# Optimization experiments

Measured on AMD Instinct MI355X. Metric: run time of the kernel, lower is better.

## Reference

```python
import jax, jax.numpy as jnp
import numpy as np

H = 16        # num_heads
NB = 64       # n_buckets
NH = 6        # n_hyperplanes = log2(NB)


def setup_inputs() -> dict:
    key = jax.random.key(0)
    k = jax.random.split(key, 6)
    E = 1024
    B, S = 2, 2048
    return {
        "x": jax.random.normal(k[0], (B, S, E), jnp.float32),
        "Wq": jax.random.normal(k[1], (E, E), jnp.float32) * (E ** -0.5),
        "bq": jax.random.normal(k[2], (E,), jnp.float32) * 0.02,
        "Wv": jax.random.normal(k[3], (E, E), jnp.float32) * (E ** -0.5),
        "bv": jax.random.normal(k[4], (E,), jnp.float32) * 0.02,
        "hyperplanes": jax.random.normal(k[5], (E // H + 1, NH), jnp.float32),
    }


def reference(x, Wq, bq, Wv, bv, hyperplanes):
    B, S, E = x.shape
    Dh = E // H
    # projections (torch Linear: x @ W.T + b)
    q = (x @ Wq.T + bq).reshape(B, S, H, Dh)
    v = (x @ Wv.T + bv).reshape(B, S, H, Dh)

    # LSH buckets from q: append a ones column, sign-project onto hyperplanes
    qa = jnp.concatenate([q, jnp.ones((B, S, H, 1), q.dtype)], axis=-1)  # [B,S,H,Dh+1]
    proj = jnp.einsum('bshe,en->bshn', qa, hyperplanes)
    bits = (proj >= 0).astype(jnp.int32)
    buckets = jnp.einsum('bshn,n->bsh', bits, 2 ** jnp.arange(NH, dtype=jnp.int32))  # [B,S,H]
    b_hs = buckets.transpose(0, 2, 1)  # [B,H,S]

    q = q.transpose(0, 2, 1, 3)  # [B,H,S,Dh]
    v = v.transpose(0, 2, 1, 3)

    # The original sums, over all NB buckets i, of (q with bucket-i tokens zeroed)
    # times its transpose. Closed form of that sum:
    #   sum_i (1-d[bs,i])(1-d[bt,i]) = NB - 2 + [bs == bt]
    scores = jnp.einsum('bhsd,bhtd->bhst', q, q) / jnp.sqrt(jnp.float32(E))
    same = (b_hs[:, :, :, None] == b_hs[:, :, None, :]).astype(scores.dtype)
    coeff = (NB - 2) + same
    attn = jax.nn.softmax(scores * coeff, axis=-1)  # [B,H,S,S]

    out = jnp.einsum('bhst,bhtd->bhsd', attn, v)
    return out.transpose(0, 2, 1, 3).reshape(B, S, E)
```

## Files before the change

kernel.cpp:

```cpp
#include <hip/hip_runtime.h>


typedef short short8 __attribute__((ext_vector_type(8)));
typedef float f32x4 __attribute__((ext_vector_type(4)));
typedef unsigned short us4 __attribute__((ext_vector_type(4)));

__device__ __forceinline__ float bff(unsigned short h) {
    return __uint_as_float(((unsigned int)h) << 16);
}
__device__ __forceinline__ unsigned short f2bf(float f) {
    unsigned int u = __float_as_uint(f);
    u += 0x7fffu + ((u >> 16) & 1u);
    return (unsigned short)(u >> 16);
}

__device__ __forceinline__ void glds16(const unsigned short* g, unsigned short* l) {
    __builtin_amdgcn_global_load_lds(
        (const __attribute__((address_space(1))) unsigned int*)g,
        (__attribute__((address_space(3))) unsigned int*)l, 16, 0, 0);
}

__global__ __launch_bounds__(256) void split_all(
    const float* __restrict__ x, const float* __restrict__ Wq,
    const float* __restrict__ Wv,
    unsigned short* __restrict__ xh, unsigned short* __restrict__ xl,
    unsigned short* __restrict__ Wqh, unsigned short* __restrict__ Wql,
    unsigned short* __restrict__ Wvh)
{
    const int blk = blockIdx.x;
    const float* in;
    unsigned short *hi, *lo;
    int idx;
    if (blk < 4096) {
        idx = blk * 256 + threadIdx.x; in = x; hi = xh; lo = xl;
    } else if (blk < 5120) {
        idx = (blk - 4096) * 256 + threadIdx.x; in = Wq; hi = Wqh; lo = Wql;
    } else {
        idx = (blk - 5120) * 256 + threadIdx.x; in = Wv; hi = Wvh; lo = nullptr;
    }
    const float4 v = ((const float4*)in)[idx];
    us4 h;
    h.x = f2bf(v.x); h.y = f2bf(v.y); h.z = f2bf(v.z); h.w = f2bf(v.w);
    ((us4*)hi)[idx] = h;
    if (lo) {
        us4 l;
        l.x = f2bf(v.x - bff(h.x)); l.y = f2bf(v.y - bff(h.y));
        l.z = f2bf(v.z - bff(h.z)); l.w = f2bf(v.w - bff(h.w));
        ((us4*)lo)[idx] = l;
    }
}

__global__ __launch_bounds__(256, 2) void gemm_qv(
    const unsigned short* __restrict__ xh, const unsigned short* __restrict__ xl,
    const unsigned short* __restrict__ wqh, const unsigned short* __restrict__ wql,
    const unsigned short* __restrict__ wvh,
    const float* __restrict__ bq, const float* __restrict__ bv,
    unsigned short* __restrict__ Qb, unsigned short* __restrict__ Qlo,
    unsigned short* __restrict__ Vt)
{
    __shared__ unsigned short Ah[128 * 64], Al[128 * 64];
    __shared__ unsigned short Bh[128 * 64], Bl[128 * 64];

    const int tid = threadIdx.x;
    const int w = tid >> 6, lane = tid & 63;
    const int i = lane & 15, qd = lane >> 4;
    const int l8 = lane >> 3, j = lane & 7;
    const int nw = w * 32;
    const int blk = blockIdx.x;
    const bool isq = blk < 256;

    f32x4 acc[8][2];
#pragma unroll
    for (int a = 0; a < 8; ++a)
#pragma unroll
        for (int b2 = 0; b2 < 2; ++b2) acc[a][b2] = f32x4{0.f, 0.f, 0.f, 0.f};

    const int gro = ((j ^ l8) << 3);

    if (isq) {
        const int m0 = (blk >> 3) * 128;
        const int n0 = (blk & 7) * 128;
        for (int k0 = 0; k0 < 1024; k0 += 64) {
            __syncthreads();
#pragma unroll
            for (int c = 0; c < 4; ++c) {
                const int r = w * 32 + c * 8;
                const size_t gx = (size_t)(m0 + r + l8) * 1024 + k0 + gro;
                const size_t gw = (size_t)(n0 + r + l8) * 1024 + k0 + gro;
                glds16(xh + gx, &Ah[r * 64]);
                glds16(xl + gx, &Al[r * 64]);
                glds16(wqh + gw, &Bh[r * 64]);
                glds16(wql + gw, &Bl[r * 64]);
            }
            __syncthreads();
#pragma unroll
            for (int kc = 0; kc < 2; ++kc) {
                const int ch = (((kc * 4 + qd) ^ (i & 7)) << 3);
                short8 bh2[2], bl2[2];
#pragma unroll
                for (int nn = 0; nn < 2; ++nn) {
                    bh2[nn] = *(const short8*)&Bh[(nw + nn * 16 + i) * 64 + ch];
                    bl2[nn] = *(const short8*)&Bl[(nw + nn * 16 + i) * 64 + ch];
                }
#pragma unroll
                for (int mm = 0; mm < 8; ++mm) {
                    const short8 ah = *(const short8*)&Ah[(mm * 16 + i) * 64 + ch];
                    const short8 al = *(const short8*)&Al[(mm * 16 + i) * 64 + ch];
#pragma unroll
                    for (int nn = 0; nn < 2; ++nn) {
                        acc[mm][nn] = __builtin_amdgcn_mfma_f32_16x16x32_bf16(
                            ah, bh2[nn], acc[mm][nn], 0, 0, 0);
                        acc[mm][nn] = __builtin_amdgcn_mfma_f32_16x16x32_bf16(
                            al, bh2[nn], acc[mm][nn], 0, 0, 0);
                        acc[mm][nn] = __builtin_amdgcn_mfma_f32_16x16x32_bf16(
                            ah, bl2[nn], acc[mm][nn], 0, 0, 0);
                    }
                }
            }
        }
#pragma unroll
        for (int mm = 0; mm < 8; ++mm)
#pragma unroll
            for (int nn = 0; nn < 2; ++nn)
#pragma unroll
                for (int rr = 0; rr < 4; ++rr) {
                    const int row = m0 + mm * 16 + qd * 4 + rr;
                    const int col = n0 + nw + nn * 16 + i;
                    const float v = acc[mm][nn][rr] + bq[col];
                    const unsigned short hs = f2bf(v);
                    const float lo = v - bff(hs);
                    const int b = row >> 11, s = row & 2047;
                    const int hh = col >> 6, d = col & 63;
                    const size_t oi = ((size_t)((b << 4) + hh) * 2048 + s) * 64 + d;
                    Qb[oi] = hs;
                    Qlo[oi] = f2bf(lo);
                }
    } else {
        const int b2 = blk - 256;
        const int m0 = (b2 & 7) * 128;
        const int n0 = (b2 >> 3) * 128;
        for (int k0 = 0; k0 < 1024; k0 += 64) {
            __syncthreads();
#pragma unroll
            for (int c = 0; c < 4; ++c) {
                const int r = w * 32 + c * 8;
                glds16(wvh + (size_t)(m0 + r + l8) * 1024 + k0 + gro, &Ah[r * 64]);
                glds16(xh + (size_t)(n0 + r + l8) * 1024 + k0 + gro, &Bh[r * 64]);
            }
            __syncthreads();
#pragma unroll
            for (int kc = 0; kc < 2; ++kc) {
                const int ch = (((kc * 4 + qd) ^ (i & 7)) << 3);
                short8 bf2[2];
#pragma unroll
                for (int nn = 0; nn < 2; ++nn)
                    bf2[nn] = *(const short8*)&Bh[(nw + nn * 16 + i) * 64 + ch];
#pragma unroll
                for (int mm = 0; mm < 8; ++mm) {
                    const short8 af = *(const short8*)&Ah[(mm * 16 + i) * 64 + ch];
#pragma unroll
                    for (int nn = 0; nn < 2; ++nn)
                        acc[mm][nn] = __builtin_amdgcn_mfma_f32_16x16x32_bf16(
                            af, bf2[nn], acc[mm][nn], 0, 0, 0);
                }
            }
        }
#pragma unroll
        for (int mm = 0; mm < 8; ++mm)
#pragma unroll
            for (int nn = 0; nn < 2; ++nn)
#pragma unroll
                for (int rr = 0; rr < 4; ++rr) {
                    const int rch = m0 + mm * 16 + qd * 4 + rr;
                    const int tok = n0 + nw + nn * 16 + i;
                    const float v = acc[mm][nn][rr] + bv[rch];
                    const int b = tok >> 11, s = tok & 2047;
                    Vt[((size_t)(b * 1024 + rch)) * 2048 + s] = f2bf(v);
                }
    }
}

__global__ __launch_bounds__(256) void bucket_kernel(
    const unsigned short* __restrict__ Qb, const unsigned short* __restrict__ Qlo,
    const float* __restrict__ hp,
    int* __restrict__ buckets, float* __restrict__ rown)
{
    __shared__ float hpl[65 * 6];
    const int tid = threadIdx.x;
    if (tid < 65 * 6) hpl[tid] = hp[tid];
    __syncthreads();

    const int idx = blockIdx.x * 256 + tid;
    const unsigned short* qh = Qb + (size_t)idx * 64;
    const unsigned short* ql = Qlo + (size_t)idx * 64;

    float pj[6];
    float nrm = 0.f;
#pragma unroll
    for (int n = 0; n < 6; ++n) pj[n] = hpl[64 * 6 + n];
    for (int d8 = 0; d8 < 8; ++d8) {
        const short8 vh = *(const short8*)(qh + d8 * 8);
        const short8 vl = *(const short8*)(ql + d8 * 8);
#pragma unroll
        for (int e = 0; e < 8; ++e) {
            const float q = bff((unsigned short)vh[e]) + bff((unsigned short)vl[e]);
            nrm = fmaf(q, q, nrm);
#pragma unroll
            for (int n = 0; n < 6; ++n)
                pj[n] = fmaf(q, hpl[(d8 * 8 + e) * 6 + n], pj[n]);
        }
    }
    int bkt = 0;
#pragma unroll
    for (int n = 0; n < 6; ++n) bkt |= (pj[n] >= 0.f) << n;
    buckets[idx] = bkt;
    rown[idx] = nrm;
}

__global__ __launch_bounds__(256, 2) void attn_kernel(
    const unsigned short* __restrict__ Qb, const unsigned short* __restrict__ Qlo,
    const unsigned short* __restrict__ Vt, const int* __restrict__ bks,
    const float* __restrict__ rown, float* __restrict__ out)
{
    __shared__ unsigned short Khi[64 * 64];
    __shared__ unsigned short Klo[64 * 64];
    __shared__ unsigned short Vs[64 * 64];
    __shared__ unsigned short P[4][16 * 64];
    __shared__ float smax[4];

    const int tid = threadIdx.x;
    const int w = tid >> 6, lane = tid & 63;
    const int i = lane & 15, qd = lane >> 4;
    const int l8 = lane >> 3, j = lane & 7;
    const int bh = blockIdx.x;
    const int qbase = blockIdx.y * 128 + w * 32;

    const unsigned short* Qh = Qb + (size_t)bh * 2048 * 64;
    const unsigned short* Ql = Qlo + (size_t)bh * 2048 * 64;
    const unsigned short* Vb = Vt + (size_t)bh * 64 * 2048;
    const int* bk = bks + bh * 2048;
    const float* rnh = rown + bh * 2048;
    unsigned short* Pw = &P[w][0];

    float lm = 0.f;
    for (int t = tid; t < 2048; t += 256) lm = fmaxf(lm, rnh[t]);
#pragma unroll
    for (int msk = 1; msk < 64; msk <<= 1) lm = fmaxf(lm, __shfl_xor(lm, msk));
    if (lane == 0) smax[w] = lm;
    __syncthreads();
    const float sqM = sqrtf(fmaxf(fmaxf(smax[0], smax[1]),
                                  fmaxf(smax[2], smax[3])));

    float m2row[2][4], lrun[2][4];
    int qbr[2][4];
#pragma unroll
    for (int ms = 0; ms < 2; ++ms)
#pragma unroll
        for (int r = 0; r < 4; ++r) {
            const int row = qbase + ms * 16 + qd * 4 + r;
            m2row[ms][r] = 2.84030586f * sqrtf(rnh[row]) * sqM + 0.72134754f;
            qbr[ms][r] = bk[row];
            lrun[ms][r] = 0.f;
        }

    short8 aqh0[2], aqh1[2], aql0[2], aql1[2];
#pragma unroll
    for (int ms = 0; ms < 2; ++ms) {
        const unsigned short* qp = Qh + (size_t)(qbase + ms * 16 + i) * 64 + qd * 8;
        const unsigned short* lp = Ql + (size_t)(qbase + ms * 16 + i) * 64 + qd * 8;
        aqh0[ms] = *(const short8*)qp; aqh1[ms] = *(const short8*)(qp + 32);
        aql0[ms] = *(const short8*)lp; aql1[ms] = *(const short8*)(lp + 32);
    }

    f32x4 o[2][4];
#pragma unroll
    for (int ms = 0; ms < 2; ++ms)
#pragma unroll
        for (int d = 0; d < 4; ++d) o[ms][d] = f32x4{0.f, 0.f, 0.f, 0.f};

    for (int t0 = 0; t0 < 2048; t0 += 64) {
        __syncthreads();
#pragma unroll
        for (int c2 = 0; c2 < 2; ++c2) {
            const int r = w * 16 + c2 * 8 + l8;
            const int swz = ((j ^ l8) << 3);
            glds16(Qh + (size_t)(t0 + r) * 64 + swz, &Khi[w * 1024 + c2 * 512]);
            glds16(Ql + (size_t)(t0 + r) * 64 + swz, &Klo[w * 1024 + c2 * 512]);
            glds16(Vb + (size_t)r * 2048 + t0 + swz, &Vs[w * 1024 + c2 * 512]);
        }
        __syncthreads();

        f32x4 s[2][4];
        int kb[4];
#pragma unroll
        for (int sub = 0; sub < 4; ++sub) {
            const int kr = sub * 16 + i;
            const int sw = i & 7;
            const short8 bh0 = *(const short8*)&Khi[kr * 64 + ((qd ^ sw) << 3)];
            const short8 bh1 = *(const short8*)&Khi[kr * 64 + (((qd + 4) ^ sw) << 3)];
            const short8 bl0 = *(const short8*)&Klo[kr * 64 + ((qd ^ sw) << 3)];
            const short8 bl1 = *(const short8*)&Klo[kr * 64 + (((qd + 4) ^ sw) << 3)];
            kb[sub] = bk[t0 + kr];
#pragma unroll
            for (int ms = 0; ms < 2; ++ms) {
                f32x4 t = f32x4{0.f, 0.f, 0.f, 0.f};
                t = __builtin_amdgcn_mfma_f32_16x16x32_bf16(aqh0[ms], bh0, t, 0, 0, 0);
                t = __builtin_amdgcn_mfma_f32_16x16x32_bf16(aqh1[ms], bh1, t, 0, 0, 0);
                t = __builtin_amdgcn_mfma_f32_16x16x32_bf16(aql0[ms], bh0, t, 0, 0, 0);
                t = __builtin_amdgcn_mfma_f32_16x16x32_bf16(aql1[ms], bh1, t, 0, 0, 0);
                t = __builtin_amdgcn_mfma_f32_16x16x32_bf16(aqh0[ms], bl0, t, 0, 0, 0);
                t = __builtin_amdgcn_mfma_f32_16x16x32_bf16(aqh1[ms], bl1, t, 0, 0, 0);
                s[ms][sub] = t;
            }
        }

        short8 vb0[4], vb1[4];
#pragma unroll
        for (int dsub = 0; dsub < 4; ++dsub) {
            const int dr = dsub * 16 + i;
            const int sw = i & 7;
            vb0[dsub] = *(const short8*)&Vs[dr * 64 + ((qd ^ sw) << 3)];
            vb1[dsub] = *(const short8*)&Vs[dr * 64 + (((qd + 4) ^ sw) << 3)];
        }

#pragma unroll
        for (int ms = 0; ms < 2; ++ms) {
#pragma unroll
            for (int sub = 0; sub < 4; ++sub)
#pragma unroll
                for (int r = 0; r < 4; ++r) {
                    const float c2f = (kb[sub] == qbr[ms][r]) ? 2.84030586f
                                                              : 2.79522164f;
                    const float p = exp2f(fmaf(s[ms][sub][r], c2f, -m2row[ms][r]));
                    lrun[ms][r] += p;
                    const unsigned int pu = __float_as_uint(p);
                    const int row = qd * 4 + r, col = sub * 16 + i;
                    Pw[row * 64 + (((col >> 3) ^ (row & 7)) << 3) + (col & 7)] =
                        (unsigned short)(pu >> 16);
                }
            const short8 pa0 = *(const short8*)&Pw[i * 64 + ((qd ^ (i & 7)) << 3)];
            const short8 pa1 = *(const short8*)&Pw[i * 64 + (((qd + 4) ^ (i & 7)) << 3)];
#pragma unroll
            for (int dsub = 0; dsub < 4; ++dsub) {
                o[ms][dsub] = __builtin_amdgcn_mfma_f32_16x16x32_bf16(
                    pa0, vb0[dsub], o[ms][dsub], 0, 0, 0);
                o[ms][dsub] = __builtin_amdgcn_mfma_f32_16x16x32_bf16(
                    pa1, vb1[dsub], o[ms][dsub], 0, 0, 0);
            }
        }
    }

#pragma unroll
    for (int ms = 0; ms < 2; ++ms)
#pragma unroll
        for (int r = 0; r < 4; ++r) {
#pragma unroll
            for (int msk = 1; msk < 16; msk <<= 1)
                lrun[ms][r] += __shfl_xor(lrun[ms][r], msk);
        }
    const int b = bh >> 4, h = bh & 15;
#pragma unroll
    for (int ms = 0; ms < 2; ++ms)
#pragma unroll
        for (int dsub = 0; dsub < 4; ++dsub)
#pragma unroll
            for (int r = 0; r < 4; ++r) {
                const float v = o[ms][dsub][r] / lrun[ms][r];
                const int srow = qbase + ms * 16 + qd * 4 + r;
                out[((size_t)(b * 2048 + srow)) * 1024 + h * 64 + dsub * 16 + i] = v;
            }
}

extern "C" void kernel_launch(void* const* d_in, const int* in_sizes, int n_in,
                              void* d_out, int out_size, void* d_ws, size_t ws_size,
                              hipStream_t stream)
{
    const float* x  = (const float*)d_in[0];
    const float* Wq = (const float*)d_in[1];
    const float* bq = (const float*)d_in[2];
    const float* Wv = (const float*)d_in[3];
    const float* bv = (const float*)d_in[4];
    const float* hp = (const float*)d_in[5];
    float* out = (float*)d_out;

    char* ws = (char*)d_ws;
    const size_t MB = (size_t)1 << 20;
    unsigned short* xh  = (unsigned short*)(ws);
    unsigned short* xl  = (unsigned short*)(ws + 8 * MB);
    unsigned short* Wqh = (unsigned short*)(ws + 16 * MB);
    unsigned short* Wql = (unsigned short*)(ws + 18 * MB);
    unsigned short* Wvh = (unsigned short*)(ws + 20 * MB);
    unsigned short* Qb  = (unsigned short*)(ws + 22 * MB);
    unsigned short* Qlo = (unsigned short*)(ws + 30 * MB);
    unsigned short* Vt  = (unsigned short*)(ws + 38 * MB);
    int*        buckets = (int*)(ws + 62 * MB);
    float*         rown = (float*)(ws + 62 * MB + 256 * 1024);

    split_all<<<dim3(6144), 256, 0, stream>>>(x, Wq, Wv, xh, xl, Wqh, Wql, Wvh);
    gemm_qv<<<dim3(512), 256, 0, stream>>>(xh, xl, Wqh, Wql, Wvh, bq, bv,
                                           Qb, Qlo, Vt);
    bucket_kernel<<<dim3(256), 256, 0, stream>>>(Qb, Qlo, hp, buckets, rown);
    attn_kernel<<<dim3(32, 16), 256, 0, stream>>>(Qb, Qlo, Vt, buckets, rown, out);
}
```

Before: 216.8 us.

## Split attention over key halves and merge partial outputs in a separate kernel

The attention kernel gains a z-dimension that splits the key range into two halves, each writing unnormalized partial outputs and row sums to workspace. A new merge kernel adds the two partials, normalizes, and writes the final layout. Because the softmax uses a precomputed per-row upper bound rather than a running max, the partials combine without rescaling. This doubles the number of blocks to improve occupancy and load balance, at the cost of extra global traffic and an extra launch.

```diff
diff --git a/kernel.cpp b/kernel.cpp
--- a/kernel.cpp
+++ b/kernel.cpp
@@ -220,7 +220,9 @@
 __global__ __launch_bounds__(256, 2) void attn_kernel(
     const unsigned short* __restrict__ Qb, const unsigned short* __restrict__ Qlo,
     const unsigned short* __restrict__ Vt, const int* __restrict__ bks,
-    const float* __restrict__ rown, float* __restrict__ out)
+    const float* __restrict__ rown,
+    float* __restrict__ op0, float* __restrict__ op1,
+    float* __restrict__ lpart)
 {
     __shared__ unsigned short Khi[64 * 64];
     __shared__ unsigned short Klo[64 * 64];
@@ -234,6 +236,8 @@
     const int l8 = lane >> 3, j = lane & 7;
     const int bh = blockIdx.x;
     const int qbase = blockIdx.y * 128 + w * 32;
+    const int half = blockIdx.z;
+    const int tbeg = half * 1024;
 
     const unsigned short* Qh = Qb + (size_t)bh * 2048 * 64;
     const unsigned short* Ql = Qlo + (size_t)bh * 2048 * 64;
@@ -241,6 +245,7 @@
     const int* bk = bks + bh * 2048;
     const float* rnh = rown + bh * 2048;
     unsigned short* Pw = &P[w][0];
+    float* op = half ? op1 : op0;
 
     float lm = 0.f;
     for (int t = tid; t < 2048; t += 256) lm = fmaxf(lm, rnh[t]);
@@ -278,7 +283,7 @@
 #pragma unroll
         for (int d = 0; d < 4; ++d) o[ms][d] = f32x4{0.f, 0.f, 0.f, 0.f};
 
-    for (int t0 = 0; t0 < 2048; t0 += 64) {
+    for (int t0 = tbeg; t0 < tbeg + 1024; t0 += 64) {
         __syncthreads();
 #pragma unroll
         for (int c2 = 0; c2 < 2; ++c2) {
@@ -358,17 +363,43 @@
             for (int msk = 1; msk < 16; msk <<= 1)
                 lrun[ms][r] += __shfl_xor(lrun[ms][r], msk);
         }
+#pragma unroll
+    for (int ms = 0; ms < 2; ++ms) {
+        if (i == 0) {
+#pragma unroll
+            for (int r = 0; r < 4; ++r) {
+                const int srow = qbase + ms * 16 + qd * 4 + r;
+                lpart[((size_t)(half * 32 + bh)) * 2048 + srow] = lrun[ms][r];
+            }
+        }
+#pragma unroll
+        for (int dsub = 0; dsub < 4; ++dsub)
+#pragma unroll
+            for (int r = 0; r < 4; ++r) {
+                const int srow = qbase + ms * 16 + qd * 4 + r;
+                op[((size_t)bh * 2048 + srow) * 64 + dsub * 16 + i] = o[ms][dsub][r];
+            }
+    }
+}
+
+__global__ __launch_bounds__(256) void merge_kernel(
+    const float* __restrict__ op0, const float* __restrict__ op1,
+    const float* __restrict__ lpart, float* __restrict__ out)
+{
+    const int idx = blockIdx.x * 256 + threadIdx.x;
+    const int d4 = idx & 15;
+    const int row = (idx >> 4) & 2047;
+    const int bh = idx >> 15;
+    const float l = lpart[(size_t)bh * 2048 + row] +
+                    lpart[(size_t)(32 + bh) * 2048 + row];
+    const float inv = 1.f / l;
+    const float4 a = ((const float4*)op0)[((size_t)bh * 2048 + row) * 16 + d4];
+    const float4 b4 = ((const float4*)op1)[((size_t)bh * 2048 + row) * 16 + d4];
+    float4 v;
+    v.x = (a.x + b4.x) * inv; v.y = (a.y + b4.y) * inv;
+    v.z = (a.z + b4.z) * inv; v.w = (a.w + b4.w) * inv;
     const int b = bh >> 4, h = bh & 15;
-#pragma unroll
-    for (int ms = 0; ms < 2; ++ms)
-#pragma unroll
-        for (int dsub = 0; dsub < 4; ++dsub)
-#pragma unroll
-            for (int r = 0; r < 4; ++r) {
-                const float v = o[ms][dsub][r] / lrun[ms][r];
-                const int srow = qbase + ms * 16 + qd * 4 + r;
-                out[((size_t)(b * 2048 + srow)) * 1024 + h * 64 + dsub * 16 + i] = v;
-            }
+    ((float4*)out)[((size_t)(b * 2048 + row)) * 256 + h * 16 + d4] = v;
 }
 
 extern "C" void kernel_launch(void* const* d_in, const int* in_sizes, int n_in,
@@ -393,6 +424,9 @@
     unsigned short* Qb  = (unsigned short*)(ws + 22 * MB);
     unsigned short* Qlo = (unsigned short*)(ws + 30 * MB);
     unsigned short* Vt  = (unsigned short*)(ws + 38 * MB);
+    float*          op0 = (float*)(ws);
+    float*          op1 = (float*)(ws + 46 * MB);
+    float*        lpart = (float*)(ws + 16 * MB);
     int*        buckets = (int*)(ws + 62 * MB);
     float*         rown = (float*)(ws + 62 * MB + 256 * 1024);
 
@@ -400,5 +434,7 @@
     gemm_qv<<<dim3(512), 256, 0, stream>>>(xh, xl, Wqh, Wql, Wvh, bq, bv,
                                            Qb, Qlo, Vt);
     bucket_kernel<<<dim3(256), 256, 0, stream>>>(Qb, Qlo, hp, buckets, rown);
-    attn_kernel<<<dim3(32, 16), 256, 0, stream>>>(Qb, Qlo, Vt, buckets, rown, out);
-}
+    attn_kernel<<<dim3(32, 16, 2), 256, 0, stream>>>(Qb, Qlo, Vt, buckets, rown,
+                                                     op0, op1, lpart);
+    merge_kernel<<<dim3(4096), 256, 0, stream>>>(op0, op1, lpart, out);
+}
```

Result: slower. 229.9 us (+6.1%).
